# Optimization experiments

Hardware: AMD Instinct MI355X
Metric: run time of the kernel (lower is better)

The kernel has to match this reference:

```python
import jax, jax.numpy as jnp
import numpy as np

N_SRC = 2_000_000
N_TAR = 2_000_000

def _make_covs(key, n):
    # 3x3 SPD block embedded in a 4x4 (last row/col zero), as in GICP covariances
    A = jax.random.normal(key, (n, 3, 3), dtype=jnp.float32)
    cov3 = 0.1 * jnp.einsum('nij,nkj->nik', A, A) + 0.1 * jnp.eye(3, dtype=jnp.float32)
    covs = jnp.zeros((n, 4, 4), dtype=jnp.float32)
    return covs.at[:, :3, :3].set(cov3)

def setup_inputs() -> dict:
    key = jax.random.key(0)
    k1, k2, k3, k4, k5, k6 = jax.random.split(key, 6)
    # homogeneous points (x, y, z, 1)
    src_xyz = jax.random.normal(k1, (N_SRC, 3), dtype=jnp.float32) * 5.0
    tar_xyz = jax.random.normal(k2, (N_TAR, 3), dtype=jnp.float32) * 5.0
    ones_s = jnp.ones((N_SRC, 1), dtype=jnp.float32)
    ones_t = jnp.ones((N_TAR, 1), dtype=jnp.float32)
    src_points = jnp.concatenate([src_xyz, ones_s], axis=1)
    tar_points = jnp.concatenate([tar_xyz, ones_t], axis=1)
    covs_src = _make_covs(k3, N_SRC)
    covs_tar = _make_covs(k4, N_TAR)
    # transformation: near-identity SE(3)-ish 4x4 (param in the original model)
    transformation = jnp.eye(4, dtype=jnp.float32) + 0.01 * jax.random.normal(k5, (4, 4), dtype=jnp.float32)
    # nearest-neighbor indices (kdtree result in the original, non-differentiable)
    nearest_indices = jax.random.randint(k6, (N_SRC,), 0, N_TAR, dtype=jnp.int64 if jax.config.jax_enable_x64 else jnp.int32)
    return {
        'transformation': transformation,
        'src_points': src_points,
        'tar_points': tar_points,
        'covs_src': covs_src,
        'covs_tar': covs_tar,
        'nearest_indices': nearest_indices,
    }

def reference(transformation, src_points, tar_points, covs_src, covs_tar, nearest_indices):
    # transformed_src_points = src_points @ T  (N,4)
    transformed_src = src_points @ transformation
    # gather KNN-matched target points / covariances
    sel_tar = tar_points[nearest_indices]          # (N,4)
    sel_covs_tar = covs_tar[nearest_indices]       # (N,4,4)
    # T @ C_src @ T^T per point
    tcov = jnp.einsum('ij,njk,lk->nil', transformation, covs_src, transformation)
    RCR = sel_covs_tar + tcov                      # (N,4,4)
    inv_RCR = jnp.linalg.inv(RCR[:, :3, :3])       # (N,3,3)
    res = sel_tar[:, :3] - transformed_src[:, :3]  # (N,3)
    maha = jnp.einsum('ni,nij,nj->n', res, inv_RCR, res)
    return 0.5 * jnp.mean(maha)
```

## Files before the change

kernel.cpp:

```cpp
#include <hip/hip_runtime.h>

#define BLOCK       256
#define UNROLL      4
#define MAX_BLOCKS  4096

__device__ __forceinline__ float gicp_point(
    int i,
    const float t00, const float t01, const float t02,
    const float t10, const float t11, const float t12,
    const float t20, const float t21, const float t22,
    const float t30, const float t31, const float t32,
    const float4* __restrict__ src, const float4* __restrict__ tar,
    const float4* __restrict__ cs,  const float4* __restrict__ ct,
    const int*    __restrict__ idx)
{
    const int    j  = idx[i];
    const float4 s  = src[i];
    const float4 tp = tar[j];

    const size_t bj = (size_t)j * 4;
    const float4 d0 = ct[bj + 0];
    const float4 d1 = ct[bj + 1];
    const float4 d2 = ct[bj + 2];

    const size_t bi = (size_t)i * 4;
    const float4 c0 = cs[bi + 0];
    const float4 c1 = cs[bi + 1];
    const float4 c2 = cs[bi + 2];

    const float ts0 = s.x * t00 + s.y * t10 + s.z * t20 + s.w * t30;
    const float ts1 = s.x * t01 + s.y * t11 + s.z * t21 + s.w * t31;
    const float ts2 = s.x * t02 + s.y * t12 + s.z * t22 + s.w * t32;
    const float r0 = tp.x - ts0;
    const float r1 = tp.y - ts1;
    const float r2 = tp.z - ts2;

    const float u00 = t00*c0.x + t01*c1.x + t02*c2.x;
    const float u01 = t00*c0.y + t01*c1.y + t02*c2.y;
    const float u02 = t00*c0.z + t01*c1.z + t02*c2.z;
    const float u10 = t10*c0.x + t11*c1.x + t12*c2.x;
    const float u11 = t10*c0.y + t11*c1.y + t12*c2.y;
    const float u12 = t10*c0.z + t11*c1.z + t12*c2.z;
    const float u20 = t20*c0.x + t21*c1.x + t22*c2.x;
    const float u21 = t20*c0.y + t21*c1.y + t22*c2.y;
    const float u22 = t20*c0.z + t21*c1.z + t22*c2.z;

    const float tc00 = u00*t00 + u01*t01 + u02*t02;
    const float tc01 = u00*t10 + u01*t11 + u02*t12;
    const float tc02 = u00*t20 + u01*t21 + u02*t22;
    const float tc11 = u10*t10 + u11*t11 + u12*t12;
    const float tc12 = u10*t20 + u11*t21 + u12*t22;
    const float tc22 = u20*t20 + u21*t21 + u22*t22;

    const float a = d0.x + tc00;
    const float b = d0.y + tc01;
    const float c = d0.z + tc02;
    const float d = d1.y + tc11;
    const float e = d1.z + tc12;
    const float f = d2.z + tc22;

    const float A00 = d * f - e * e;
    const float A01 = c * e - b * f;
    const float A02 = b * e - c * d;
    const float A11 = a * f - c * c;
    const float A12 = b * c - a * e;
    const float A22 = a * d - b * b;

    const float det = a * A00 + b * A01 + c * A02;

    const float num = r0 * r0 * A00 + r1 * r1 * A11 + r2 * r2 * A22
                    + 2.0f * (r0 * r1 * A01 + r0 * r2 * A02 + r1 * r2 * A12);

    return num / det;
}

__global__ __launch_bounds__(BLOCK) void gicp_maha_kernel(
    const float*  __restrict__ T,
    const float4* __restrict__ src,
    const float4* __restrict__ tar,
    const float4* __restrict__ cs,
    const float4* __restrict__ ct,
    const int*    __restrict__ idx,
    float*        __restrict__ partial,
    int n)
{
    const float t00 = T[0],  t01 = T[1],  t02 = T[2];
    const float t10 = T[4],  t11 = T[5],  t12 = T[6];
    const float t20 = T[8],  t21 = T[9],  t22 = T[10];
    const float t30 = T[12], t31 = T[13], t32 = T[14];

    const int stride = gridDim.x * BLOCK;
    const int step   = stride * UNROLL;

    float local = 0.0f;
    for (int base = blockIdx.x * BLOCK + threadIdx.x; base < n; base += step) {
        if (base + 3 * stride < n) {
            float v0 = gicp_point(base,            t00,t01,t02,t10,t11,t12,t20,t21,t22,t30,t31,t32, src,tar,cs,ct,idx);
            float v1 = gicp_point(base +   stride, t00,t01,t02,t10,t11,t12,t20,t21,t22,t30,t31,t32, src,tar,cs,ct,idx);
            float v2 = gicp_point(base + 2*stride, t00,t01,t02,t10,t11,t12,t20,t21,t22,t30,t31,t32, src,tar,cs,ct,idx);
            float v3 = gicp_point(base + 3*stride, t00,t01,t02,t10,t11,t12,t20,t21,t22,t30,t31,t32, src,tar,cs,ct,idx);
            local += (v0 + v1) + (v2 + v3);
        } else {
            #pragma unroll
            for (int k = 0; k < UNROLL; ++k) {
                int i = base + k * stride;
                const float m = (i < n) ? 1.0f : 0.0f;
                i = (i < n) ? i : (n - 1);
                local += m * gicp_point(i, t00,t01,t02,t10,t11,t12,t20,t21,t22,t30,t31,t32, src,tar,cs,ct,idx);
            }
        }
    }

    for (int off = 32; off > 0; off >>= 1)
        local += __shfl_down(local, off, 64);

    __shared__ float wsum[BLOCK / 64];
    const int wave = threadIdx.x >> 6;
    if ((threadIdx.x & 63) == 0) wsum[wave] = local;
    __syncthreads();
    if (threadIdx.x == 0) {
        float s = wsum[0];
        #pragma unroll
        for (int w = 1; w < BLOCK / 64; ++w) s += wsum[w];
        partial[blockIdx.x] = s;
    }
}

__global__ __launch_bounds__(256) void gicp_finalize_kernel(
    const float* __restrict__ partial, float* __restrict__ out,
    double scale, int nblocks)
{
    double s = 0.0;
    for (int k = threadIdx.x; k < nblocks; k += 256)
        s += (double)partial[k];
    for (int off = 32; off > 0; off >>= 1)
        s += __shfl_down(s, off, 64);
    __shared__ double wsum[4];
    const int wave = threadIdx.x >> 6;
    if ((threadIdx.x & 63) == 0) wsum[wave] = s;
    __syncthreads();
    if (threadIdx.x == 0)
        out[0] = (float)((wsum[0] + wsum[1] + wsum[2] + wsum[3]) * scale);
}

extern "C" void kernel_launch(void* const* d_in, const int* in_sizes, int n_in,
                              void* d_out, int out_size, void* d_ws, size_t ws_size,
                              hipStream_t stream) {
    const float*  T   = (const float*)d_in[0];
    const float4* src = (const float4*)d_in[1];
    const float4* tar = (const float4*)d_in[2];
    const float4* cs  = (const float4*)d_in[3];
    const float4* ct  = (const float4*)d_in[4];
    const int*    idx = (const int*)d_in[5];
    const int n = in_sizes[1] / 4;

    int nblocks = (n + BLOCK * UNROLL - 1) / (BLOCK * UNROLL);
    if (nblocks < 1) nblocks = 1;
    if (nblocks > MAX_BLOCKS) nblocks = MAX_BLOCKS;
    const int ws_cap = (int)(ws_size / sizeof(float));
    if (nblocks > ws_cap) nblocks = ws_cap;

    float* partial = (float*)d_ws;

    gicp_maha_kernel<<<nblocks, BLOCK, 0, stream>>>(T, src, tar, cs, ct,
                                                    idx, partial, n);
    gicp_finalize_kernel<<<1, 256, 0, stream>>>(partial, (float*)d_out,
                                                0.5 / (double)n, nblocks);
}
```

Baseline: 341.8 us.

## Stage covariance loads through LDS with cooperative global_load_lds per wave

```diff
diff --git a/kernel.cpp b/kernel.cpp
--- a/kernel.cpp
+++ b/kernel.cpp
@@ -1,77 +1,15 @@
 #include <hip/hip_runtime.h>
+#include <stdint.h>
 
 #define BLOCK       256
-#define UNROLL      4
+#define WPB         (BLOCK / 64)
 #define MAX_BLOCKS  4096
 
-__device__ __forceinline__ float gicp_point(
-    int i,
-    const float t00, const float t01, const float t02,
-    const float t10, const float t11, const float t12,
-    const float t20, const float t21, const float t22,
-    const float t30, const float t31, const float t32,
-    const float4* __restrict__ src, const float4* __restrict__ tar,
-    const float4* __restrict__ cs,  const float4* __restrict__ ct,
-    const int*    __restrict__ idx)
-{
-    const int    j  = idx[i];
-    const float4 s  = src[i];
-    const float4 tp = tar[j];
+typedef __attribute__((address_space(3))) uint32_t       lds_u32;
+typedef __attribute__((address_space(1))) const uint32_t glb_u32;
 
-    const size_t bj = (size_t)j * 4;
-    const float4 d0 = ct[bj + 0];
-    const float4 d1 = ct[bj + 1];
-    const float4 d2 = ct[bj + 2];
-
-    const size_t bi = (size_t)i * 4;
-    const float4 c0 = cs[bi + 0];
-    const float4 c1 = cs[bi + 1];
-    const float4 c2 = cs[bi + 2];
-
-    const float ts0 = s.x * t00 + s.y * t10 + s.z * t20 + s.w * t30;
-    const float ts1 = s.x * t01 + s.y * t11 + s.z * t21 + s.w * t31;
-    const float ts2 = s.x * t02 + s.y * t12 + s.z * t22 + s.w * t32;
-    const float r0 = tp.x - ts0;
-    const float r1 = tp.y - ts1;
-    const float r2 = tp.z - ts2;
-
-    const float u00 = t00*c0.x + t01*c1.x + t02*c2.x;
-    const float u01 = t00*c0.y + t01*c1.y + t02*c2.y;
-    const float u02 = t00*c0.z + t01*c1.z + t02*c2.z;
-    const float u10 = t10*c0.x + t11*c1.x + t12*c2.x;
-    const float u11 = t10*c0.y + t11*c1.y + t12*c2.y;
-    const float u12 = t10*c0.z + t11*c1.z + t12*c2.z;
-    const float u20 = t20*c0.x + t21*c1.x + t22*c2.x;
-    const float u21 = t20*c0.y + t21*c1.y + t22*c2.y;
-    const float u22 = t20*c0.z + t21*c1.z + t22*c2.z;
-
-    const float tc00 = u00*t00 + u01*t01 + u02*t02;
-    const float tc01 = u00*t10 + u01*t11 + u02*t12;
-    const float tc02 = u00*t20 + u01*t21 + u02*t22;
-    const float tc11 = u10*t10 + u11*t11 + u12*t12;
-    const float tc12 = u10*t20 + u11*t21 + u12*t22;
-    const float tc22 = u20*t20 + u21*t21 + u22*t22;
-
-    const float a = d0.x + tc00;
-    const float b = d0.y + tc01;
-    const float c = d0.z + tc02;
-    const float d = d1.y + tc11;
-    const float e = d1.z + tc12;
-    const float f = d2.z + tc22;
-
-    const float A00 = d * f - e * e;
-    const float A01 = c * e - b * f;
-    const float A02 = b * e - c * d;
-    const float A11 = a * f - c * c;
-    const float A12 = b * c - a * e;
-    const float A22 = a * d - b * b;
-
-    const float det = a * A00 + b * A01 + c * A02;
-
-    const float num = r0 * r0 * A00 + r1 * r1 * A11 + r2 * r2 * A22
-                    + 2.0f * (r0 * r1 * A01 + r0 * r2 * A02 + r1 * r2 * A12);
-
-    return num / det;
+__device__ __forceinline__ void coop_load16(const void* gptr, void* lds_uniform_base) {
+    __builtin_amdgcn_global_load_lds((glb_u32*)gptr, (lds_u32*)lds_uniform_base, 16, 0, 0);
 }
 
 __global__ __launch_bounds__(BLOCK) void gicp_maha_kernel(
@@ -82,47 +20,119 @@
     const float4* __restrict__ ct,
     const int*    __restrict__ idx,
     float*        __restrict__ partial,
-    int n)
+    int n, int nbatches)
 {
+    __shared__ float4 stage[WPB][2][256];
+
+    const int lane   = threadIdx.x & 63;
+    const int wv     = threadIdx.x >> 6;
+    const int gwave  = blockIdx.x * WPB + wv;
+    const int nwaves = gridDim.x * WPB;
+
     const float t00 = T[0],  t01 = T[1],  t02 = T[2];
     const float t10 = T[4],  t11 = T[5],  t12 = T[6];
     const float t20 = T[8],  t21 = T[9],  t22 = T[10];
     const float t30 = T[12], t31 = T[13], t32 = T[14];
 
-    const int stride = gridDim.x * BLOCK;
-    const int step   = stride * UNROLL;
+    float4* const st_cs = &stage[wv][0][0];
+    float4* const st_ct = &stage[wv][1][0];
 
     float local = 0.0f;
-    for (int base = blockIdx.x * BLOCK + threadIdx.x; base < n; base += step) {
-        if (base + 3 * stride < n) {
-            float v0 = gicp_point(base,            t00,t01,t02,t10,t11,t12,t20,t21,t22,t30,t31,t32, src,tar,cs,ct,idx);
-            float v1 = gicp_point(base +   stride, t00,t01,t02,t10,t11,t12,t20,t21,t22,t30,t31,t32, src,tar,cs,ct,idx);
-            float v2 = gicp_point(base + 2*stride, t00,t01,t02,t10,t11,t12,t20,t21,t22,t30,t31,t32, src,tar,cs,ct,idx);
-            float v3 = gicp_point(base + 3*stride, t00,t01,t02,t10,t11,t12,t20,t21,t22,t30,t31,t32, src,tar,cs,ct,idx);
-            local += (v0 + v1) + (v2 + v3);
-        } else {
-            #pragma unroll
-            for (int k = 0; k < UNROLL; ++k) {
-                int i = base + k * stride;
-                const float m = (i < n) ? 1.0f : 0.0f;
-                i = (i < n) ? i : (n - 1);
-                local += m * gicp_point(i, t00,t01,t02,t10,t11,t12,t20,t21,t22,t30,t31,t32, src,tar,cs,ct,idx);
-            }
+
+    for (int b = gwave; b < nbatches; b += nwaves) {
+        const int base = b * 64;
+        int i = base + lane;
+        const float msk = (i < n) ? 1.0f : 0.0f;
+        i = (i < n) ? i : (n - 1);
+
+        const int    j  = idx[i];
+        const float4 s  = src[i];
+        const float4 tp = tar[j];
+
+        const char* const cs_bytes = (const char*)cs;
+        #pragma unroll
+        for (int g = 0; g < 4; ++g) {
+            int q = base + g * 16 + (lane >> 2);
+            q = (q < n) ? q : (n - 1);
+            const void* gp = cs_bytes + (size_t)q * 64 + (size_t)(lane & 3) * 16;
+            coop_load16(gp, (char*)st_cs + g * 1024);
         }
+
+        const char* const ct_bytes = (const char*)ct;
+        #pragma unroll
+        for (int g = 0; g < 4; ++g) {
+            const int jg = __shfl(j, (lane >> 2) + g * 16, 64);
+            const void* gp = ct_bytes + (size_t)jg * 64 + (size_t)(lane & 3) * 16;
+            coop_load16(gp, (char*)st_ct + g * 1024);
+        }
+
+        asm volatile("s_waitcnt vmcnt(0)" ::: "memory");
+        __builtin_amdgcn_sched_barrier(0);
+
+        const float4 c0 = st_cs[lane * 4 + 0];
+        const float4 c1 = st_cs[lane * 4 + 1];
+        const float4 c2 = st_cs[lane * 4 + 2];
+        const float4 d0 = st_ct[lane * 4 + 0];
+        const float4 d1 = st_ct[lane * 4 + 1];
+        const float4 d2 = st_ct[lane * 4 + 2];
+
+        const float ts0 = s.x * t00 + s.y * t10 + s.z * t20 + s.w * t30;
+        const float ts1 = s.x * t01 + s.y * t11 + s.z * t21 + s.w * t31;
+        const float ts2 = s.x * t02 + s.y * t12 + s.z * t22 + s.w * t32;
+        const float r0 = tp.x - ts0;
+        const float r1 = tp.y - ts1;
+        const float r2 = tp.z - ts2;
+
+        const float u00 = t00*c0.x + t01*c1.x + t02*c2.x;
+        const float u01 = t00*c0.y + t01*c1.y + t02*c2.y;
+        const float u02 = t00*c0.z + t01*c1.z + t02*c2.z;
+        const float u10 = t10*c0.x + t11*c1.x + t12*c2.x;
+        const float u11 = t10*c0.y + t11*c1.y + t12*c2.y;
+        const float u12 = t10*c0.z + t11*c1.z + t12*c2.z;
+        const float u20 = t20*c0.x + t21*c1.x + t22*c2.x;
+        const float u21 = t20*c0.y + t21*c1.y + t22*c2.y;
+        const float u22 = t20*c0.z + t21*c1.z + t22*c2.z;
+
+        const float tc00 = u00*t00 + u01*t01 + u02*t02;
+        const float tc01 = u00*t10 + u01*t11 + u02*t12;
+        const float tc02 = u00*t20 + u01*t21 + u02*t22;
+        const float tc11 = u10*t10 + u11*t11 + u12*t12;
+        const float tc12 = u10*t20 + u11*t21 + u12*t22;
+        const float tc22 = u20*t20 + u21*t21 + u22*t22;
+
+        const float a = d0.x + tc00;
+        const float bb = d0.y + tc01;
+        const float c = d0.z + tc02;
+        const float d = d1.y + tc11;
+        const float e = d1.z + tc12;
+        const float f = d2.z + tc22;
+
+        const float A00 = d * f - e * e;
+        const float A01 = c * e - bb * f;
+        const float A02 = bb * e - c * d;
+        const float A11 = a * f - c * c;
+        const float A12 = bb * c - a * e;
+        const float A22 = a * d - bb * bb;
+
+        const float det = a * A00 + bb * A01 + c * A02;
+
+        const float num = r0 * r0 * A00 + r1 * r1 * A11 + r2 * r2 * A22
+                        + 2.0f * (r0 * r1 * A01 + r0 * r2 * A02 + r1 * r2 * A12);
+
+        local += msk * (num / det);
     }
 
     for (int off = 32; off > 0; off >>= 1)
         local += __shfl_down(local, off, 64);
 
-    __shared__ float wsum[BLOCK / 64];
-    const int wave = threadIdx.x >> 6;
-    if ((threadIdx.x & 63) == 0) wsum[wave] = local;
+    __shared__ float wsum[WPB];
+    if ((threadIdx.x & 63) == 0) wsum[wv] = local;
     __syncthreads();
     if (threadIdx.x == 0) {
-        float s = wsum[0];
+        float ssum = wsum[0];
         #pragma unroll
-        for (int w = 1; w < BLOCK / 64; ++w) s += wsum[w];
-        partial[blockIdx.x] = s;
+        for (int w = 1; w < WPB; ++w) ssum += wsum[w];
+        partial[blockIdx.x] = ssum;
     }
 }
 
@@ -154,7 +164,8 @@
     const int*    idx = (const int*)d_in[5];
     const int n = in_sizes[1] / 4;
 
-    int nblocks = (n + BLOCK * UNROLL - 1) / (BLOCK * UNROLL);
+    const int nbatches = (n + 63) / 64;
+    int nblocks = (nbatches + WPB * 4 - 1) / (WPB * 4);
     if (nblocks < 1) nblocks = 1;
     if (nblocks > MAX_BLOCKS) nblocks = MAX_BLOCKS;
     const int ws_cap = (int)(ws_size / sizeof(float));
@@ -162,8 +173,8 @@
 
     float* partial = (float*)d_ws;
 
-    gicp_maha_kernel<<<nblocks, BLOCK, 0, stream>>>(T, src, tar, cs, ct,
-                                                    idx, partial, n);
+    gicp_maha_kernel<<<nblocks, BLOCK, 0, stream>>>(T, src, tar, cs, ct, idx,
+                                                    partial, n, nbatches);
     gicp_finalize_kernel<<<1, 256, 0, stream>>>(partial, (float*)d_out,
                                                 0.5 / (double)n, nblocks);
 }
```

Result: faster. 334.1 us (-2.2%).

## Prefetch gathered target arrays into LLC and stream source data nontemporally

Applied to the files above, without the earlier changes.

```diff
diff --git a/kernel.cpp b/kernel.cpp
--- a/kernel.cpp
+++ b/kernel.cpp
@@ -1,8 +1,24 @@
 #include <hip/hip_runtime.h>
+#include <stdint.h>
 
-#define BLOCK       256
-#define UNROLL      4
-#define MAX_BLOCKS  4096
+#define BLOCK        256
+#define UNROLL       4
+#define MAX_BLOCKS   4096
+#define WARM_BLOCKS  2048
+
+typedef float f32x4 __attribute__((ext_vector_type(4)));
+
+__global__ __launch_bounds__(256) void llc_warm_kernel(
+    const float* __restrict__ tar, long ntar_f,
+    const float* __restrict__ ct,  long nct_f)
+{
+    const long stride = (long)gridDim.x * 256 * 32;
+    const long base   = ((long)blockIdx.x * 256 + threadIdx.x) * 32;
+    float acc = 0.0f;
+    for (long k = base; k < nct_f; k += stride)  acc += ct[k];
+    for (long k = base; k < ntar_f; k += stride) acc += tar[k];
+    asm volatile("" :: "v"(acc));
+}
 
 __device__ __forceinline__ float gicp_point(
     int i,
@@ -10,23 +26,23 @@
     const float t10, const float t11, const float t12,
     const float t20, const float t21, const float t22,
     const float t30, const float t31, const float t32,
-    const float4* __restrict__ src, const float4* __restrict__ tar,
-    const float4* __restrict__ cs,  const float4* __restrict__ ct,
-    const int*    __restrict__ idx)
+    const f32x4* __restrict__ src, const f32x4* __restrict__ tar,
+    const f32x4* __restrict__ cs,  const f32x4* __restrict__ ct,
+    const int*   __restrict__ idx)
 {
-    const int    j  = idx[i];
-    const float4 s  = src[i];
-    const float4 tp = tar[j];
+    const int   j  = __builtin_nontemporal_load(&idx[i]);
+    const f32x4 s  = __builtin_nontemporal_load(&src[i]);
+    const f32x4 tp = tar[j];
 
     const size_t bj = (size_t)j * 4;
-    const float4 d0 = ct[bj + 0];
-    const float4 d1 = ct[bj + 1];
-    const float4 d2 = ct[bj + 2];
+    const f32x4 d0 = ct[bj + 0];
+    const f32x4 d1 = ct[bj + 1];
+    const f32x4 d2 = ct[bj + 2];
 
     const size_t bi = (size_t)i * 4;
-    const float4 c0 = cs[bi + 0];
-    const float4 c1 = cs[bi + 1];
-    const float4 c2 = cs[bi + 2];
+    const f32x4 c0 = __builtin_nontemporal_load(&cs[bi + 0]);
+    const f32x4 c1 = __builtin_nontemporal_load(&cs[bi + 1]);
+    const f32x4 c2 = __builtin_nontemporal_load(&cs[bi + 2]);
 
     const float ts0 = s.x * t00 + s.y * t10 + s.z * t20 + s.w * t30;
     const float ts1 = s.x * t01 + s.y * t11 + s.z * t21 + s.w * t31;
@@ -75,13 +91,13 @@
 }
 
 __global__ __launch_bounds__(BLOCK) void gicp_maha_kernel(
-    const float*  __restrict__ T,
-    const float4* __restrict__ src,
-    const float4* __restrict__ tar,
-    const float4* __restrict__ cs,
-    const float4* __restrict__ ct,
-    const int*    __restrict__ idx,
-    float*        __restrict__ partial,
+    const float* __restrict__ T,
+    const f32x4* __restrict__ src,
+    const f32x4* __restrict__ tar,
+    const f32x4* __restrict__ cs,
+    const f32x4* __restrict__ ct,
+    const int*   __restrict__ idx,
+    float*       __restrict__ partial,
     int n)
 {
     const float t00 = T[0],  t01 = T[1],  t02 = T[2];
@@ -146,13 +162,16 @@
 extern "C" void kernel_launch(void* const* d_in, const int* in_sizes, int n_in,
                               void* d_out, int out_size, void* d_ws, size_t ws_size,
                               hipStream_t stream) {
-    const float*  T   = (const float*)d_in[0];
-    const float4* src = (const float4*)d_in[1];
-    const float4* tar = (const float4*)d_in[2];
-    const float4* cs  = (const float4*)d_in[3];
-    const float4* ct  = (const float4*)d_in[4];
-    const int*    idx = (const int*)d_in[5];
+    const float* T   = (const float*)d_in[0];
+    const f32x4* src = (const f32x4*)d_in[1];
+    const f32x4* tar = (const f32x4*)d_in[2];
+    const f32x4* cs  = (const f32x4*)d_in[3];
+    const f32x4* ct  = (const f32x4*)d_in[4];
+    const int*   idx = (const int*)d_in[5];
     const int n = in_sizes[1] / 4;
+
+    const long ntar_f = (long)(in_sizes[2]);
+    const long nct_f  = (long)(in_sizes[4]);
 
     int nblocks = (n + BLOCK * UNROLL - 1) / (BLOCK * UNROLL);
     if (nblocks < 1) nblocks = 1;
@@ -162,8 +181,10 @@
 
     float* partial = (float*)d_ws;
 
-    gicp_maha_kernel<<<nblocks, BLOCK, 0, stream>>>(T, src, tar, cs, ct,
-                                                    idx, partial, n);
+    llc_warm_kernel<<<WARM_BLOCKS, 256, 0, stream>>>(
+        (const float*)tar, ntar_f, (const float*)ct, nct_f);
+    gicp_maha_kernel<<<nblocks, BLOCK, 0, stream>>>(T, src, tar, cs, ct, idx,
+                                                    partial, n);
     gicp_finalize_kernel<<<1, 256, 0, stream>>>(partial, (float*)d_out,
                                                 0.5 / (double)n, nblocks);
 }
```

After: 378.3 us. 10.7% more time.
